# Performance work log

Hardware: AMD Instinct MI355X
Metric: run time of the kernel (lower is better)

Reference implementation:

```python
import jax, jax.numpy as jnp
from jax import lax
import numpy as np

N, C_IN, C_OUT, H, W_SP = 16, 16, 64, 256, 256
K, STRIDE, PAD = 3, 1, 1


def setup_inputs() -> dict:
    key = jax.random.key(0)
    k1, k2 = jax.random.split(key)
    x = jax.random.normal(k1, (N, C_IN, H, W_SP), dtype=jnp.float32)
    # One 3x3 filter per output channel (C_out independent Super0Net branches),
    # stacked into a single OIHW weight -> equivalent to the concatenated loop.
    W = jax.random.normal(k2, (C_OUT, C_IN, K, K), dtype=jnp.float32) * 0.05
    return {"x": x, "W": W}


def reference(x, W):
    # Fused form of: for ch in range(C_out): conv_ch(x) ; concat(dim=1).
    # Each branch is a Conv2d(C_in, 1, 3, stride=1, padding=1, bias=False).
    return lax.conv_general_dilated(
        x, W,
        window_strides=(STRIDE, STRIDE),
        padding=((PAD, PAD), (PAD, PAD)),
        dimension_numbers=("NCHW", "OIHW", "NCHW"),
    )
```

## Files before the change

kernel.cpp:

```cpp
#include <hip/hip_runtime.h>
#include <hip/hip_bf16.h>

typedef __attribute__((ext_vector_type(8))) __bf16 bf16x8;
typedef __attribute__((ext_vector_type(4))) float f32x4;

constexpr int CI_ = 16, CO_ = 64, H_ = 256, W_ = 256;
constexpr int WTROW = 168;

__global__ void transform_x_kernel(const float* __restrict__ x,
                                   unsigned short* __restrict__ xt) {
  int idx = blockIdx.x * 256 + threadIdx.x;
  int w = idx & 255;
  int h = (idx >> 8) & 255;
  int n = idx >> 16;
  const float* src = x + (((size_t)n * CI_) * H_ + h) * W_ + w;
  unsigned short tmp[16];
#pragma unroll
  for (int ci = 0; ci < 16; ++ci) {
    float v = src[(size_t)ci * (H_ * W_)];
    __bf16 b = (__bf16)v;
    tmp[ci] = __builtin_bit_cast(unsigned short, b);
  }
  uint4* dst = (uint4*)(xt + (size_t)idx * 16);
  dst[0] = ((uint4*)tmp)[0];
  dst[1] = ((uint4*)tmp)[1];
}

__global__ void transform_w_kernel(const float* __restrict__ Wg,
                                   unsigned short* __restrict__ wt) {
  int idx = blockIdx.x * 256 + threadIdx.x;
  int co = idx / WTROW;
  int kk = idx - co * WTROW;
  float v = 0.f;
  if (kk < 144) {
    int t = kk >> 4;
    int ci = kk & 15;
    v = Wg[(co * 16 + ci) * 9 + t];
  }
  __bf16 b = (__bf16)v;
  wt[idx] = __builtin_bit_cast(unsigned short, b);
}

__global__ __launch_bounds__(256) void conv_mfma_kernel(
    const unsigned short* __restrict__ xt, const unsigned short* __restrict__ wt,
    float* __restrict__ out) {
  __shared__ unsigned short xs[3][258][16];
  __shared__ unsigned short wlds[CO_][WTROW];

  int tid = threadIdx.x;
  int bid = blockIdx.x;
  int h = bid & 255;
  int n = bid >> 8;

  {
    const uint4* src = (const uint4*)wt;
    uint4* dst = (uint4*)&wlds[0][0];
    for (int c = tid; c < 1344; c += 256) dst[c] = src[c];
  }
  {
    const uint4* srcbase = (const uint4*)xt;
    for (int c = tid; c < 1536; c += 256) {
      int r = c >> 9;
      int off = c & 511;
      int hh = h - 1 + r;
      uint4 v = make_uint4(0u, 0u, 0u, 0u);
      if (hh >= 0 && hh < 256)
        v = srcbase[(size_t)(n * 256 + hh) * 512 + off];
      *(uint4*)(&xs[r][1][0] + off * 8) = v;
    }
    if (tid < 6) {
      int r = tid >> 1;
      int wp = (tid & 1) ? 257 : 0;
      *(uint4*)&xs[r][wp][0] = make_uint4(0u, 0u, 0u, 0u);
      *(uint4*)&xs[r][wp][8] = make_uint4(0u, 0u, 0u, 0u);
    }
  }
  __syncthreads();

  int lane = tid & 63;
  int wave = tid >> 6;
  int col = lane & 15;
  int g = lane >> 4;

  f32x4 acc[4][4];
#pragma unroll
  for (int i = 0; i < 4; ++i)
#pragma unroll
    for (int j = 0; j < 4; ++j) acc[i][j] = (f32x4){0.f, 0.f, 0.f, 0.f};

  int pxb = wave * 64 + col;

#pragma unroll
  for (int s = 0; s < 5; ++s) {
    bf16x8 a[4];
#pragma unroll
    for (int cb = 0; cb < 4; ++cb)
      a[cb] = *(const bf16x8*)&wlds[cb * 16 + col][s * 32 + 8 * g];

    int tap = 2 * s + (g >> 1);
    if (tap > 8) tap = 8;
    int kh = tap / 3;
    int kw = tap - kh * 3;
    int ci0 = (g & 1) * 8;

    bf16x8 b[4];
#pragma unroll
    for (int pb = 0; pb < 4; ++pb)
      b[pb] = *(const bf16x8*)&xs[kh][pxb + pb * 16 + kw][ci0];

#pragma unroll
    for (int cb = 0; cb < 4; ++cb)
#pragma unroll
      for (int pb = 0; pb < 4; ++pb)
        acc[cb][pb] = __builtin_amdgcn_mfma_f32_16x16x32_bf16(
            a[cb], b[pb], acc[cb][pb], 0, 0, 0);
  }

  size_t obase = ((size_t)n * CO_ * H_ + h) * W_;
#pragma unroll
  for (int cb = 0; cb < 4; ++cb) {
#pragma unroll
    for (int r = 0; r < 4; ++r) {
      int co = cb * 16 + g * 4 + r;
      float* dst = out + obase + (size_t)co * (H_ * W_);
#pragma unroll
      for (int pb = 0; pb < 4; ++pb) dst[pxb + pb * 16] = acc[cb][pb][r];
    }
  }
}

extern "C" void kernel_launch(void* const* d_in, const int* in_sizes, int n_in,
                              void* d_out, int out_size, void* d_ws, size_t ws_size,
                              hipStream_t stream) {
  const float* x = (const float*)d_in[0];
  const float* W = (const float*)d_in[1];
  float* out = (float*)d_out;

  unsigned short* xt = (unsigned short*)d_ws;
  unsigned short* wt = xt + (size_t)16 * 256 * 256 * 16;

  transform_x_kernel<<<4096, 256, 0, stream>>>(x, xt);
  transform_w_kernel<<<42, 256, 0, stream>>>(W, wt);
  conv_mfma_kernel<<<4096, 256, 0, stream>>>(xt, wt, out);
}
```

Baseline: 336.5 us.

## Vectorize transforms and output stores, swizzle LDS input tile

The input transform kernel now has each thread handle four pixels, using float4 loads and eight 16-byte stores, and launches a quarter of the blocks. The conv kernel remaps each lane to four consecutive pixels so the output can be written as one 16-byte float4 store per channel instead of four scalar stores. The LDS input tile gets an XOR swizzle to avoid bank conflicts on the new strided B-operand reads. This targets memory-bound global store and load traffic, at the cost of extra address arithmetic.

After: 343.5 us. +2.1%, slower.

```diff
diff --git a/kernel.cpp b/kernel.cpp
--- a/kernel.cpp
+++ b/kernel.cpp
@@ -6,24 +6,32 @@
 
 constexpr int CI_ = 16, CO_ = 64, H_ = 256, W_ = 256;
 constexpr int WTROW = 168;
+constexpr int RSZ = 258 * 32;
+
+__device__ __forceinline__ unsigned swz(unsigned o) {
+  return o ^ (((o >> 7) & 7u) << 4);
+}
 
 __global__ void transform_x_kernel(const float* __restrict__ x,
                                    unsigned short* __restrict__ xt) {
-  int idx = blockIdx.x * 256 + threadIdx.x;
-  int w = idx & 255;
-  int h = (idx >> 8) & 255;
-  int n = idx >> 16;
-  const float* src = x + (((size_t)n * CI_) * H_ + h) * W_ + w;
-  unsigned short tmp[16];
+  int t = blockIdx.x * 256 + threadIdx.x;
+  int p0 = t << 2;
+  int w = p0 & 255;
+  int h = (p0 >> 8) & 255;
+  int n = p0 >> 16;
+  const float* src = x + ((size_t)n * CI_) * (H_ * W_) + h * W_ + w;
+  unsigned short tmp[64];
 #pragma unroll
   for (int ci = 0; ci < 16; ++ci) {
-    float v = src[(size_t)ci * (H_ * W_)];
-    __bf16 b = (__bf16)v;
-    tmp[ci] = __builtin_bit_cast(unsigned short, b);
+    float4 v = *(const float4*)(src + (size_t)ci * (H_ * W_));
+    tmp[0 * 16 + ci] = __builtin_bit_cast(unsigned short, (__bf16)v.x);
+    tmp[1 * 16 + ci] = __builtin_bit_cast(unsigned short, (__bf16)v.y);
+    tmp[2 * 16 + ci] = __builtin_bit_cast(unsigned short, (__bf16)v.z);
+    tmp[3 * 16 + ci] = __builtin_bit_cast(unsigned short, (__bf16)v.w);
   }
-  uint4* dst = (uint4*)(xt + (size_t)idx * 16);
-  dst[0] = ((uint4*)tmp)[0];
-  dst[1] = ((uint4*)tmp)[1];
+  uint4* dst = (uint4*)(xt + (size_t)p0 * 16);
+#pragma unroll
+  for (int q = 0; q < 8; ++q) dst[q] = ((const uint4*)tmp)[q];
 }
 
 __global__ void transform_w_kernel(const float* __restrict__ Wg,
@@ -37,14 +45,13 @@
     int ci = kk & 15;
     v = Wg[(co * 16 + ci) * 9 + t];
   }
-  __bf16 b = (__bf16)v;
-  wt[idx] = __builtin_bit_cast(unsigned short, b);
+  wt[idx] = __builtin_bit_cast(unsigned short, (__bf16)v);
 }
 
 __global__ __launch_bounds__(256) void conv_mfma_kernel(
     const unsigned short* __restrict__ xt, const unsigned short* __restrict__ wt,
     float* __restrict__ out) {
-  __shared__ unsigned short xs[3][258][16];
+  __shared__ unsigned char xs[3 * RSZ];
   __shared__ unsigned short wlds[CO_][WTROW];
 
   int tid = threadIdx.x;
@@ -61,18 +68,18 @@
     const uint4* srcbase = (const uint4*)xt;
     for (int c = tid; c < 1536; c += 256) {
       int r = c >> 9;
-      int off = c & 511;
+      int j = c & 511;
       int hh = h - 1 + r;
       uint4 v = make_uint4(0u, 0u, 0u, 0u);
       if (hh >= 0 && hh < 256)
-        v = srcbase[(size_t)(n * 256 + hh) * 512 + off];
-      *(uint4*)(&xs[r][1][0] + off * 8) = v;
+        v = srcbase[(size_t)(n * 256 + hh) * 512 + j];
+      *(uint4*)(xs + r * RSZ + swz(32u + 16u * (unsigned)j)) = v;
     }
-    if (tid < 6) {
-      int r = tid >> 1;
-      int wp = (tid & 1) ? 257 : 0;
-      *(uint4*)&xs[r][wp][0] = make_uint4(0u, 0u, 0u, 0u);
-      *(uint4*)&xs[r][wp][8] = make_uint4(0u, 0u, 0u, 0u);
+    if (tid < 12) {
+      int r = tid >> 2;
+      int q = tid & 3;
+      unsigned off = ((q >> 1) ? 257u * 32u : 0u) + (q & 1) * 16u;
+      *(uint4*)(xs + r * RSZ + swz(off)) = make_uint4(0u, 0u, 0u, 0u);
     }
   }
   __syncthreads();
@@ -88,7 +95,7 @@
 #pragma unroll
     for (int j = 0; j < 4; ++j) acc[i][j] = (f32x4){0.f, 0.f, 0.f, 0.f};
 
-  int pxb = wave * 64 + col;
+  int pxb = wave * 64 + 4 * col;
 
 #pragma unroll
   for (int s = 0; s < 5; ++s) {
@@ -105,8 +112,10 @@
 
     bf16x8 b[4];
 #pragma unroll
-    for (int pb = 0; pb < 4; ++pb)
-      b[pb] = *(const bf16x8*)&xs[kh][pxb + pb * 16 + kw][ci0];
+    for (int pb = 0; pb < 4; ++pb) {
+      unsigned wp = (unsigned)(pxb + pb + kw);
+      b[pb] = *(const bf16x8*)(xs + kh * RSZ + swz(wp * 32u + ci0 * 2u));
+    }
 
 #pragma unroll
     for (int cb = 0; cb < 4; ++cb)
@@ -116,15 +125,14 @@
             a[cb], b[pb], acc[cb][pb], 0, 0, 0);
   }
 
-  size_t obase = ((size_t)n * CO_ * H_ + h) * W_;
+  size_t obase = ((size_t)n * CO_ * H_ + h) * W_ + pxb;
 #pragma unroll
   for (int cb = 0; cb < 4; ++cb) {
 #pragma unroll
     for (int r = 0; r < 4; ++r) {
       int co = cb * 16 + g * 4 + r;
-      float* dst = out + obase + (size_t)co * (H_ * W_);
-#pragma unroll
-      for (int pb = 0; pb < 4; ++pb) dst[pxb + pb * 16] = acc[cb][pb][r];
+      f32x4 v = {acc[cb][0][r], acc[cb][1][r], acc[cb][2][r], acc[cb][3][r]};
+      *(f32x4*)(out + obase + (size_t)co * (H_ * W_)) = v;
     }
   }
 }
@@ -139,7 +147,7 @@
   unsigned short* xt = (unsigned short*)d_ws;
   unsigned short* wt = xt + (size_t)16 * 256 * 256 * 16;
 
-  transform_x_kernel<<<4096, 256, 0, stream>>>(x, xt);
+  transform_x_kernel<<<1024, 256, 0, stream>>>(x, xt);
   transform_w_kernel<<<42, 256, 0, stream>>>(W, wt);
   conv_mfma_kernel<<<4096, 256, 0, stream>>>(xt, wt, out);
 }
```
